# Kernel optimization log

Measured on AMD Instinct MI355X. Metric: run time of the kernel, lower is better.

Reference implementation:

```python
import jax, jax.numpy as jnp
import numpy as np

GAMMA = 0.98
LBDA = 0.93
EPSI = 0.2
NUM_ACTIONS = 6


def future_returns(rewards, dones, values, gamma):
    # rewards, values: [B, T] float; dones: [B, T] bool
    last = jnp.where(dones[:, -1], rewards[:, -1], values[:, -1])  # Rs[:, T-1]

    def step(carry, xs):
        r_t, d_t = xs
        nv = jnp.where(d_t, jnp.zeros_like(carry), carry)
        R = r_t + gamma * nv
        return R, R

    # time-major inputs for t = 0..T-2, scanned in reverse (t = T-2 .. 0)
    xs = (rewards[:, :-1].T, dones[:, :-1].T)
    _, Rs_head = jax.lax.scan(step, last, xs, reverse=True)  # [T-1, B]
    return jnp.concatenate([Rs_head.T, last[:, None]], axis=1)  # [B, T]


def generalized_advantage(rewards, dones, values, gamma, lbda):
    next_values = jnp.where(dones[:, :-1], 0.0, values[:, 1:])
    td_err = rewards[:, :-1] + gamma * next_values - values[:, :-1]  # [B, T-1]

    def step(gae, xs):
        td_t, d_t = xs
        gae = jnp.where(d_t, jnp.zeros_like(gae), gae)
        gae = td_t + gamma * lbda * gae
        return gae, gae

    xs = (td_err.T, dones[:, :-1].T)
    init = jnp.zeros_like(td_err[:, -1])
    _, A = jax.lax.scan(step, init, xs, reverse=True)  # [T-1, B]
    return A.T  # [B, T-1]


def setup_inputs() -> dict:
    key = jax.random.key(0)
    k1, k2, k3, k4, k5, k6 = jax.random.split(key, 6)
    B, T = 2048, 1024
    rewards = jax.random.normal(k1, (B, T), dtype=jnp.float32)
    values = jax.random.normal(k2, (B, T), dtype=jnp.float32)
    logits = jax.random.normal(k3, (B, T, NUM_ACTIONS), dtype=jnp.float32)
    logits_old = jax.random.normal(k4, (B, T, NUM_ACTIONS), dtype=jnp.float32)
    dones = jax.random.randint(k5, (B, T), 0, 2).astype(jnp.bool_)
    actions = jax.random.randint(k6, (B, T), 0, NUM_ACTIONS, dtype=jnp.int32)
    return {"rewards": rewards, "values": values, "logits": logits,
            "logits_old": logits_old, "dones": dones, "actions": actions}


def reference(rewards, values, logits, logits_old, dones, actions):
    sg = jax.lax.stop_gradient
    log_probs = jax.nn.log_softmax(logits, axis=-1)
    log_probs_old = jax.nn.log_softmax(logits_old, axis=-1)

    V = sg(values)  # values_trainable.detach()
    Rs = sg(future_returns(rewards, dones, V, GAMMA))          # [B, T]
    A = generalized_advantage(rewards, dones, V, GAMMA, LBDA)  # [B, T-1]

    # one-hot einsum == gather of chosen-action log-probs
    log_pis = jnp.take_along_axis(log_probs, actions[..., None], axis=-1)[..., 0]
    log_pis_old = jnp.take_along_axis(log_probs_old, actions[..., None], axis=-1)[..., 0]

    r = jnp.exp(log_pis - sg(log_pis_old))[:, :-1]
    # faithful to torch.clip(min=1-eps, max=eps): min applied then max -> constant eps
    r_clipped = jnp.clip(r, 1.0 - EPSI, EPSI)

    ppo_loss = -jnp.minimum(r * A, r_clipped * A).mean()
    value_loss = jnp.square(sg(Rs) - values).mean()
    entropy_loss = -log_pis.mean()
    return jnp.stack([ppo_loss, value_loss, entropy_loss])  # [3]
```

## Files before the change

### kernel.cpp

```cpp
#include <hip/hip_runtime.h>
#include <math.h>

#define GAMMA 0.98f
#define LBDA  0.93f
#define GL    (GAMMA * LBDA)
constexpr int B  = 2048;
constexpr int T  = 1024;
constexpr int NT = B * T;
constexpr int NBLK_E = NT / 2 / 256;

__device__ __forceinline__ float logpi(float x0, float x1, float x2,
                                       float x3, float x4, float x5, int a) {
    float m = fmaxf(fmaxf(fmaxf(x0, x1), fmaxf(x2, x3)), fmaxf(x4, x5));
    float s = __expf(x0 - m) + __expf(x1 - m) + __expf(x2 - m) +
              __expf(x3 - m) + __expf(x4 - m) + __expf(x5 - m);
    float lse = m + __logf(s);
    float r = x0;
    r = (a == 1) ? x1 : r;
    r = (a == 2) ? x2 : r;
    r = (a == 3) ? x3 : r;
    r = (a == 4) ? x4 : r;
    r = (a == 5) ? x5 : r;
    return r - lse;
}

__device__ __forceinline__ int sw(int m) { return m ^ ((m >> 3) & 7); }

__global__ __launch_bounds__(256) void k_elem(
        const float4* __restrict__ lg, const float4* __restrict__ lgo,
        const int2* __restrict__ act, float2* __restrict__ rbuf,
        float* __restrict__ part_e) {
    int tid = threadIdx.x;
    int p = blockIdx.x * 256 + tid;
    const float4* s0 = lg  + blockIdx.x * 768;
    const float4* s1 = lgo + blockIdx.x * 768;

    float4 g0 = s0[tid], g1 = s0[tid + 256], g2 = s0[tid + 512];
    float4 h0 = s1[tid], h1 = s1[tid + 256], h2 = s1[tid + 512];
    int2 aa = act[p];

    __shared__ float4 sb[768];
    sb[sw(tid)] = g0; sb[sw(tid + 256)] = g1; sb[sw(tid + 512)] = g2;
    __syncthreads();
    float4 A0 = sb[sw(3 * tid)], A1 = sb[sw(3 * tid + 1)], A2 = sb[sw(3 * tid + 2)];
    float lp0 = logpi(A0.x, A0.y, A0.z, A0.w, A1.x, A1.y, aa.x);
    float lp1 = logpi(A1.z, A1.w, A2.x, A2.y, A2.z, A2.w, aa.y);
    __syncthreads();

    sb[sw(tid)] = h0; sb[sw(tid + 256)] = h1; sb[sw(tid + 512)] = h2;
    __syncthreads();
    float4 B0 = sb[sw(3 * tid)], B1 = sb[sw(3 * tid + 1)], B2 = sb[sw(3 * tid + 2)];
    float lpo0 = logpi(B0.x, B0.y, B0.z, B0.w, B1.x, B1.y, aa.x);
    float lpo1 = logpi(B1.z, B1.w, B2.x, B2.y, B2.z, B2.w, aa.y);

    rbuf[p] = make_float2(__expf(lp0 - lpo0), __expf(lp1 - lpo1));

    float es = lp0 + lp1;
    #pragma unroll
    for (int d = 32; d; d >>= 1) es += __shfl_xor(es, d);
    __shared__ float sm[4];
    int lane = tid & 63;
    if (lane == 0) sm[tid >> 6] = es;
    __syncthreads();
    if (tid == 0) part_e[blockIdx.x] = sm[0] + sm[1] + sm[2] + sm[3];
}

__global__ __launch_bounds__(256) void k_scan(
        const float4* __restrict__ rw4, const float4* __restrict__ vl4,
        const int4* __restrict__ dn4, const float4* __restrict__ rr4,
        float* __restrict__ part_v, float* __restrict__ part_p) {
    int j = threadIdx.x;
    int base = blockIdx.x * 256 + j;
    float4 rw = rw4[base], vl = vl4[base], rr = rr4[base];
    int4 dn = dn4[base];

    __shared__ float sv[256];
    __shared__ float wa1[4], wb1[4], wa2[4], wb2[4];
    __shared__ float red[8];

    sv[j] = vl.x;
    __syncthreads();
    float vnext = (j < 255) ? sv[j + 1] : 0.0f;

    float rwk[4] = {rw.x, rw.y, rw.z, rw.w};
    float vk[5]  = {vl.x, vl.y, vl.z, vl.w, vnext};
    int   dk[4]  = {dn.x, dn.y, dn.z, dn.w};

    float b1[4], c1[4], b2[4], c2[4];
    #pragma unroll
    for (int k = 0; k < 4; ++k) {
        bool d = dk[k] != 0;
        c1[k] = d ? 0.0f : GAMMA;
        b1[k] = rwk[k];
        c2[k] = d ? 0.0f : GL;
        b2[k] = rwk[k] + (d ? 0.0f : GAMMA * vk[k + 1]) - vk[k];
    }
    if (j == 255) {
        b1[3] = dk[3] ? rwk[3] : vk[3];
        c1[3] = 0.0f;
        b2[3] = 0.0f;
        c2[3] = 0.0f;
    }

    float a1 = 1.0f, bb1 = 0.0f, a2 = 1.0f, bb2 = 0.0f;
    #pragma unroll
    for (int k = 3; k >= 0; --k) {
        bb1 = b1[k] + c1[k] * bb1;  a1 = c1[k] * a1;
        bb2 = b2[k] + c2[k] * bb2;  a2 = c2[k] * a2;
    }

    int lane = j & 63, wv = j >> 6;
    #pragma unroll
    for (int d = 1; d < 64; d <<= 1) {
        float an1 = __shfl_down(a1, d), bn1 = __shfl_down(bb1, d);
        float an2 = __shfl_down(a2, d), bn2 = __shfl_down(bb2, d);
        if (lane + d < 64) {
            bb1 = a1 * bn1 + bb1;  a1 = a1 * an1;
            bb2 = a2 * bn2 + bb2;  a2 = a2 * an2;
        }
    }
    if (lane == 0) { wa1[wv] = a1; wb1[wv] = bb1; wa2[wv] = a2; wb2[wv] = bb2; }
    float a1s = __shfl_down(a1, 1), b1s = __shfl_down(bb1, 1);
    float a2s = __shfl_down(a2, 1), b2s = __shfl_down(bb2, 1);
    __syncthreads();

    float x1 = 0.0f, x2 = 0.0f;
    for (int w2 = 3; w2 > wv; --w2) {
        x1 = wa1[w2] * x1 + wb1[w2];
        x2 = wa2[w2] * x2 + wb2[w2];
    }
    float cin1 = (lane == 63) ? x1 : (a1s * x1 + b1s);
    float cin2 = (lane == 63) ? x2 : (a2s * x2 + b2s);

    float rrk[4] = {rr.x, rr.y, rr.z, rr.w};
    float vsum = 0.0f, psum = 0.0f;
    float R = cin1, A = cin2;
    #pragma unroll
    for (int k = 3; k >= 0; --k) {
        R = b1[k] + c1[k] * R;
        float dv = R - vk[k];
        vsum += dv * dv;
        A = b2[k] + c2[k] * A;
        if (4 * j + k < T - 1) {
            psum += fminf(rrk[k] * A, 0.2f * A);
        }
    }

    #pragma unroll
    for (int d = 32; d; d >>= 1) {
        vsum += __shfl_xor(vsum, d);
        psum += __shfl_xor(psum, d);
    }
    if (lane == 0) { red[wv] = vsum; red[4 + wv] = psum; }
    __syncthreads();
    if (j == 0) {
        part_v[blockIdx.x] = red[0] + red[1] + red[2] + red[3];
        part_p[blockIdx.x] = red[4] + red[5] + red[6] + red[7];
    }
}

__global__ __launch_bounds__(256) void k_fin(
        const float* __restrict__ part_e, const float* __restrict__ part_v,
        const float* __restrict__ part_p, float* __restrict__ out) {
    int tid = threadIdx.x;
    float e = 0.0f, v = 0.0f, p = 0.0f;
    for (int i = tid; i < NBLK_E; i += 256) e += part_e[i];
    for (int i = tid; i < B; i += 256)      v += part_v[i];
    for (int i = tid; i < B; i += 256)      p += part_p[i];
    #pragma unroll
    for (int d = 32; d; d >>= 1) {
        e += __shfl_xor(e, d);
        v += __shfl_xor(v, d);
        p += __shfl_xor(p, d);
    }
    __shared__ float sm[12];
    int lane = tid & 63, wv = tid >> 6;
    if (lane == 0) { sm[wv] = e; sm[4 + wv] = v; sm[8 + wv] = p; }
    __syncthreads();
    if (tid == 0) {
        float te = sm[0] + sm[1] + sm[2] + sm[3];
        float tv = sm[4] + sm[5] + sm[6] + sm[7];
        float tp = sm[8] + sm[9] + sm[10] + sm[11];
        out[0] = -tp / (float)(B * (T - 1));
        out[1] =  tv / (float)(B * T);
        out[2] = -te / (float)(B * T);
    }
}

extern "C" void kernel_launch(void* const* d_in, const int* in_sizes, int n_in,
                              void* d_out, int out_size, void* d_ws, size_t ws_size,
                              hipStream_t stream) {
    const float* rewards    = (const float*)d_in[0];
    const float* values     = (const float*)d_in[1];
    const float* logits     = (const float*)d_in[2];
    const float* logits_old = (const float*)d_in[3];
    const int*   dones      = (const int*)d_in[4];
    const int*   actions    = (const int*)d_in[5];

    float* rbuf   = (float*)d_ws;
    float* part_e = rbuf + NT;
    float* part_v = part_e + NBLK_E;
    float* part_p = part_v + B;

    k_elem<<<NBLK_E, 256, 0, stream>>>(
        (const float4*)logits, (const float4*)logits_old,
        (const int2*)actions, (float2*)rbuf, part_e);

    k_scan<<<B, 256, 0, stream>>>(
        (const float4*)rewards, (const float4*)values,
        (const int4*)dones, (const float4*)rbuf, part_v, part_p);

    k_fin<<<1, 256, 0, stream>>>(part_e, part_v, part_p, (float*)d_out);
}
```

Baseline: 166.7 us.

## Fuse log-softmax ratio kernel into per-row scan kernel

Merges the elementwise log-prob kernel and the per-row reverse scan kernel into one kernel with one 512-thread block per batch row, where each thread handles two timesteps. The probability ratio is computed in registers and used directly in the scan, so the B*T float intermediate buffer is no longer written and read back through global memory, and one kernel launch is removed. In exchange each block holds more shared memory (24KB logits staging) and there are fewer, larger blocks, which may reduce occupancy.

Measured after the change: 156.0 us. 1.07x faster.

```diff
diff --git a/kernel.cpp b/kernel.cpp
--- a/kernel.cpp
+++ b/kernel.cpp
@@ -6,8 +6,6 @@
 #define GL    (GAMMA * LBDA)
 constexpr int B  = 2048;
 constexpr int T  = 1024;
-constexpr int NT = B * T;
-constexpr int NBLK_E = NT / 2 / 256;
 
 __device__ __forceinline__ float logpi(float x0, float x1, float x2,
                                        float x3, float x4, float x5, int a) {
@@ -26,85 +24,68 @@
 
 __device__ __forceinline__ int sw(int m) { return m ^ ((m >> 3) & 7); }
 
-__global__ __launch_bounds__(256) void k_elem(
-        const float4* __restrict__ lg, const float4* __restrict__ lgo,
-        const int2* __restrict__ act, float2* __restrict__ rbuf,
-        float* __restrict__ part_e) {
-    int tid = threadIdx.x;
-    int p = blockIdx.x * 256 + tid;
-    const float4* s0 = lg  + blockIdx.x * 768;
-    const float4* s1 = lgo + blockIdx.x * 768;
-
-    float4 g0 = s0[tid], g1 = s0[tid + 256], g2 = s0[tid + 512];
-    float4 h0 = s1[tid], h1 = s1[tid + 256], h2 = s1[tid + 512];
-    int2 aa = act[p];
-
-    __shared__ float4 sb[768];
-    sb[sw(tid)] = g0; sb[sw(tid + 256)] = g1; sb[sw(tid + 512)] = g2;
-    __syncthreads();
-    float4 A0 = sb[sw(3 * tid)], A1 = sb[sw(3 * tid + 1)], A2 = sb[sw(3 * tid + 2)];
+__global__ __launch_bounds__(512) void k_fused(
+        const float2* __restrict__ rw2, const float2* __restrict__ vl2,
+        const int2* __restrict__ dn2, const int2* __restrict__ ac2,
+        const float4* __restrict__ lg4, const float4* __restrict__ lgo4,
+        float* __restrict__ part_e, float* __restrict__ part_v,
+        float* __restrict__ part_p) {
+    int j = threadIdx.x;
+    int b = blockIdx.x;
+
+    const float4* Lrow = lg4  + (size_t)b * 1536;
+    const float4* Orow = lgo4 + (size_t)b * 1536;
+    int rbase = b * 512 + j;
+
+    float4 g0 = Lrow[j], g1 = Lrow[j + 512], g2 = Lrow[j + 1024];
+    float4 h0 = Orow[j], h1 = Orow[j + 512], h2 = Orow[j + 1024];
+    float2 rw = rw2[rbase], vl = vl2[rbase];
+    int2 dn = dn2[rbase], aa = ac2[rbase];
+
+    __shared__ float4 sb[1536];
+    __shared__ float sv[512];
+    __shared__ float wa1[8], wb1[8], wa2[8], wb2[8];
+    __shared__ float red[24];
+
+    sv[j] = vl.x;
+    sb[sw(j)] = g0; sb[sw(j + 512)] = g1; sb[sw(j + 1024)] = g2;
+    __syncthreads();
+    float4 A0 = sb[sw(3 * j)], A1 = sb[sw(3 * j + 1)], A2 = sb[sw(3 * j + 2)];
+    float vnext = (j < 511) ? sv[j + 1] : 0.0f;
     float lp0 = logpi(A0.x, A0.y, A0.z, A0.w, A1.x, A1.y, aa.x);
     float lp1 = logpi(A1.z, A1.w, A2.x, A2.y, A2.z, A2.w, aa.y);
     __syncthreads();
-
-    sb[sw(tid)] = h0; sb[sw(tid + 256)] = h1; sb[sw(tid + 512)] = h2;
-    __syncthreads();
-    float4 B0 = sb[sw(3 * tid)], B1 = sb[sw(3 * tid + 1)], B2 = sb[sw(3 * tid + 2)];
+    sb[sw(j)] = h0; sb[sw(j + 512)] = h1; sb[sw(j + 1024)] = h2;
+    __syncthreads();
+    float4 B0 = sb[sw(3 * j)], B1 = sb[sw(3 * j + 1)], B2 = sb[sw(3 * j + 2)];
     float lpo0 = logpi(B0.x, B0.y, B0.z, B0.w, B1.x, B1.y, aa.x);
     float lpo1 = logpi(B1.z, B1.w, B2.x, B2.y, B2.z, B2.w, aa.y);
 
-    rbuf[p] = make_float2(__expf(lp0 - lpo0), __expf(lp1 - lpo1));
-
-    float es = lp0 + lp1;
-    #pragma unroll
-    for (int d = 32; d; d >>= 1) es += __shfl_xor(es, d);
-    __shared__ float sm[4];
-    int lane = tid & 63;
-    if (lane == 0) sm[tid >> 6] = es;
-    __syncthreads();
-    if (tid == 0) part_e[blockIdx.x] = sm[0] + sm[1] + sm[2] + sm[3];
-}
-
-__global__ __launch_bounds__(256) void k_scan(
-        const float4* __restrict__ rw4, const float4* __restrict__ vl4,
-        const int4* __restrict__ dn4, const float4* __restrict__ rr4,
-        float* __restrict__ part_v, float* __restrict__ part_p) {
-    int j = threadIdx.x;
-    int base = blockIdx.x * 256 + j;
-    float4 rw = rw4[base], vl = vl4[base], rr = rr4[base];
-    int4 dn = dn4[base];
-
-    __shared__ float sv[256];
-    __shared__ float wa1[4], wb1[4], wa2[4], wb2[4];
-    __shared__ float red[8];
-
-    sv[j] = vl.x;
-    __syncthreads();
-    float vnext = (j < 255) ? sv[j + 1] : 0.0f;
-
-    float rwk[4] = {rw.x, rw.y, rw.z, rw.w};
-    float vk[5]  = {vl.x, vl.y, vl.z, vl.w, vnext};
-    int   dk[4]  = {dn.x, dn.y, dn.z, dn.w};
-
-    float b1[4], c1[4], b2[4], c2[4];
-    #pragma unroll
-    for (int k = 0; k < 4; ++k) {
+    float rr0 = __expf(lp0 - lpo0), rr1 = __expf(lp1 - lpo1);
+
+    float rwk[2] = {rw.x, rw.y};
+    float vk[3]  = {vl.x, vl.y, vnext};
+    int   dk[2]  = {dn.x, dn.y};
+
+    float b1[2], c1[2], b2[2], c2[2];
+    #pragma unroll
+    for (int k = 0; k < 2; ++k) {
         bool d = dk[k] != 0;
         c1[k] = d ? 0.0f : GAMMA;
         b1[k] = rwk[k];
         c2[k] = d ? 0.0f : GL;
         b2[k] = rwk[k] + (d ? 0.0f : GAMMA * vk[k + 1]) - vk[k];
     }
-    if (j == 255) {
-        b1[3] = dk[3] ? rwk[3] : vk[3];
-        c1[3] = 0.0f;
-        b2[3] = 0.0f;
-        c2[3] = 0.0f;
+    if (j == 511) {
+        b1[1] = dk[1] ? rwk[1] : vk[1];
+        c1[1] = 0.0f;
+        b2[1] = 0.0f;
+        c2[1] = 0.0f;
     }
 
     float a1 = 1.0f, bb1 = 0.0f, a2 = 1.0f, bb2 = 0.0f;
     #pragma unroll
-    for (int k = 3; k >= 0; --k) {
+    for (int k = 1; k >= 0; --k) {
         bb1 = b1[k] + c1[k] * bb1;  a1 = c1[k] * a1;
         bb2 = b2[k] + c2[k] * bb2;  a2 = c2[k] * a2;
     }
@@ -125,37 +106,45 @@
     __syncthreads();
 
     float x1 = 0.0f, x2 = 0.0f;
-    for (int w2 = 3; w2 > wv; --w2) {
+    for (int w2 = 7; w2 > wv; --w2) {
         x1 = wa1[w2] * x1 + wb1[w2];
         x2 = wa2[w2] * x2 + wb2[w2];
     }
     float cin1 = (lane == 63) ? x1 : (a1s * x1 + b1s);
     float cin2 = (lane == 63) ? x2 : (a2s * x2 + b2s);
 
-    float rrk[4] = {rr.x, rr.y, rr.z, rr.w};
+    float rrk[2] = {rr0, rr1};
     float vsum = 0.0f, psum = 0.0f;
     float R = cin1, A = cin2;
     #pragma unroll
-    for (int k = 3; k >= 0; --k) {
+    for (int k = 1; k >= 0; --k) {
         R = b1[k] + c1[k] * R;
         float dv = R - vk[k];
         vsum += dv * dv;
         A = b2[k] + c2[k] * A;
-        if (4 * j + k < T - 1) {
+        if (2 * j + k < T - 1) {
             psum += fminf(rrk[k] * A, 0.2f * A);
         }
     }
+    float es = lp0 + lp1;
 
     #pragma unroll
     for (int d = 32; d; d >>= 1) {
+        es   += __shfl_xor(es, d);
         vsum += __shfl_xor(vsum, d);
         psum += __shfl_xor(psum, d);
     }
-    if (lane == 0) { red[wv] = vsum; red[4 + wv] = psum; }
+    if (lane == 0) { red[wv] = es; red[8 + wv] = vsum; red[16 + wv] = psum; }
     __syncthreads();
     if (j == 0) {
-        part_v[blockIdx.x] = red[0] + red[1] + red[2] + red[3];
-        part_p[blockIdx.x] = red[4] + red[5] + red[6] + red[7];
+        float te = 0.0f, tv = 0.0f, tp = 0.0f;
+        #pragma unroll
+        for (int w2 = 0; w2 < 8; ++w2) {
+            te += red[w2]; tv += red[8 + w2]; tp += red[16 + w2];
+        }
+        part_e[b] = te;
+        part_v[b] = tv;
+        part_p[b] = tp;
     }
 }
 
@@ -164,9 +153,11 @@
         const float* __restrict__ part_p, float* __restrict__ out) {
     int tid = threadIdx.x;
     float e = 0.0f, v = 0.0f, p = 0.0f;
-    for (int i = tid; i < NBLK_E; i += 256) e += part_e[i];
-    for (int i = tid; i < B; i += 256)      v += part_v[i];
-    for (int i = tid; i < B; i += 256)      p += part_p[i];
+    for (int i = tid; i < B; i += 256) {
+        e += part_e[i];
+        v += part_v[i];
+        p += part_p[i];
+    }
     #pragma unroll
     for (int d = 32; d; d >>= 1) {
         e += __shfl_xor(e, d);
@@ -197,18 +188,15 @@
     const int*   dones      = (const int*)d_in[4];
     const int*   actions    = (const int*)d_in[5];
 
-    float* rbuf   = (float*)d_ws;
-    float* part_e = rbuf + NT;
-    float* part_v = part_e + NBLK_E;
+    float* part_e = (float*)d_ws;
+    float* part_v = part_e + B;
     float* part_p = part_v + B;
 
-    k_elem<<<NBLK_E, 256, 0, stream>>>(
+    k_fused<<<B, 512, 0, stream>>>(
+        (const float2*)rewards, (const float2*)values,
+        (const int2*)dones, (const int2*)actions,
         (const float4*)logits, (const float4*)logits_old,
-        (const int2*)actions, (float2*)rbuf, part_e);
-
-    k_scan<<<B, 256, 0, stream>>>(
-        (const float4*)rewards, (const float4*)values,
-        (const int4*)dones, (const float4*)rbuf, part_v, part_p);
+        part_e, part_v, part_p);
 
     k_fin<<<1, 256, 0, stream>>>(part_e, part_v, part_p, (float*)d_out);
 }
```
